# Performance work log

Hardware: AMD Instinct MI355X
Metric: run time of the kernel (lower is better)

## Reference

```python
import jax, jax.numpy as jnp
import numpy as np

B, S, D, H = 2, 2048, 1024, 16
DK = D // H


def setup_inputs() -> dict:
    key = jax.random.key(0)
    ks = jax.random.split(key, 7)
    x = jax.random.normal(ks[0], (B, S, D), dtype=jnp.float32)
    gamma = jax.random.normal(ks[1], (D,), dtype=jnp.float32)
    mask = jax.random.randint(ks[2], (B, S), 0, 2, dtype=jnp.int32)
    w_qkv_w = jax.random.normal(ks[3], (D, 3 * D), dtype=jnp.float32) / np.sqrt(D)
    w_qkv_b = jax.random.normal(ks[4], (3 * D,), dtype=jnp.float32) * 0.02
    w_o_w = jax.random.normal(ks[5], (D, D), dtype=jnp.float32) / np.sqrt(D)
    w_o_b = jax.random.normal(ks[6], (D,), dtype=jnp.float32) * 0.02
    return {"x": x, "gamma": gamma, "mask": mask, "w_qkv_w": w_qkv_w,
            "w_qkv_b": w_qkv_b, "w_o_w": w_o_w, "w_o_b": w_o_b}


def reference(x, gamma, mask, w_qkv_w, w_qkv_b, w_o_w, w_o_b):
    b, s, d = x.shape
    # QKV projection, then per-head interleaved chunk (matches torch view+chunk)
    qkv = x @ w_qkv_w + w_qkv_b                      # [B,S,3D]
    qkv = qkv.reshape(b, s, H, 3 * DK).transpose(0, 2, 1, 3)  # [B,H,S,3*dk]
    q, k, v = jnp.split(qkv, 3, axis=-1)             # each [B,H,S,dk]
    scale = 1.0 / np.sqrt(DK).astype(np.float32)
    scores = jnp.einsum('bhqd,bhkd->bhqk', q, k) * scale  # [B,H,S,S]
    m = mask[:, None, None, :]                       # 2D mask -> [B,1,1,S]
    scores = jnp.where(m == 0, -jnp.inf, scores)
    attn = jax.nn.softmax(scores, axis=-1)           # dropout p=0.0 -> identity
    out = jnp.einsum('bhqk,bhkd->bhqd', attn, v)     # [B,H,S,dk]
    out = out.transpose(0, 2, 1, 3).reshape(b, s, d) # [B,S,D]
    out = out @ w_o_w + w_o_b
    return (gamma + 1.0) * out
```

## Files before the change

### kernel.cpp

```cpp
#include <hip/hip_runtime.h>
#include <hip/hip_bf16.h>


using bf16 = __hip_bfloat16;
typedef __attribute__((ext_vector_type(8))) short bf16x8;
typedef __attribute__((ext_vector_type(4))) float f32x4;

#define QSCALE 0.18033688011112042f

static __device__ __forceinline__ f32x4 mfma_bf16(bf16x8 a, bf16x8 b, f32x4 c) {
    return __builtin_amdgcn_mfma_f32_16x16x32_bf16(a, b, c, 0, 0, 0);
}

static __device__ __forceinline__ void gld_lds16(const void* g, void* s) {
    __builtin_amdgcn_global_load_lds(
        (const __attribute__((address_space(1))) unsigned int*)g,
        (__attribute__((address_space(3))) unsigned int*)s,
        16, 0, 0);
}

static __device__ __forceinline__ short f2s(float f) {
    bf16 h = __float2bfloat16(f);
    return *reinterpret_cast<short*>(&h);
}

__global__ void prep_kernel(const float* __restrict__ x, bf16* __restrict__ xb,
                            const float* __restrict__ wqkv, bf16* __restrict__ wqkvT,
                            const float* __restrict__ wo, bf16* __restrict__ woT) {
    __shared__ float tile[32][33];
    int blk = blockIdx.x;
    if (blk < 4096) {
        int i = blk * 256 + threadIdx.x;
        float4 f = reinterpret_cast<const float4*>(x)[i];
        xb[4*i+0] = __float2bfloat16(f.x);
        xb[4*i+1] = __float2bfloat16(f.y);
        xb[4*i+2] = __float2bfloat16(f.z);
        xb[4*i+3] = __float2bfloat16(f.w);
        return;
    }
    const float* in; bf16* out; int R, C, bx, by;
    if (blk < 7168) {
        int idx = blk - 4096; in = wqkv; out = wqkvT; R = 1024; C = 3072;
        bx = idx % 96; by = idx / 96;
    } else {
        int idx = blk - 7168; in = wo; out = woT; R = 1024; C = 1024;
        bx = idx & 31; by = idx >> 5;
    }
    int c0 = bx * 32, r0 = by * 32;
    int xo = threadIdx.x & 31, yo = threadIdx.x >> 5;
#pragma unroll
    for (int i = 0; i < 32; i += 8) tile[yo + i][xo] = in[(size_t)(r0 + yo + i) * C + c0 + xo];
    __syncthreads();
#pragma unroll
    for (int i = 0; i < 32; i += 8)
        out[(size_t)(c0 + yo + i) * R + r0 + xo] = __float2bfloat16(tile[xo][yo + i]);
}

__global__ void transpose_v_kernel(const bf16* __restrict__ in, bf16* __restrict__ out) {
    __shared__ bf16 t[64][72];
    const int bh = blockIdx.y, s0 = blockIdx.x * 64;
    const int r = threadIdx.x >> 2, c16 = (threadIdx.x & 3) * 16;
    const uint4* src = (const uint4*)(in + ((size_t)bh * 2048 + s0 + r) * 64 + c16);
    uint4 a0 = src[0], a1 = src[1];
    *(uint4*)&t[r][c16] = a0;
    *(uint4*)&t[r][c16 + 8] = a1;
    __syncthreads();
    bf16 tmp[16];
#pragma unroll
    for (int ii = 0; ii < 16; ++ii) {
        int i = c16 + ii;
        int a = i >> 5, rem = i & 31, q = rem >> 3, jj = rem & 7;
        int sp = a * 32 + q * 4 + (jj < 4 ? jj : 16 + jj - 4);
        tmp[ii] = t[sp][r];
    }
    uint4* dst = (uint4*)(out + ((size_t)bh * 64 + r) * 2048 + s0 + c16);
    dst[0] = ((uint4*)tmp)[0];
    dst[1] = ((uint4*)tmp)[1];
}

template <int EPI, int TM, int MINW>
__global__ __launch_bounds__(256, MINW)
void gemm_bt_kernel(const bf16* __restrict__ A, const bf16* __restrict__ Bt,
                    int M, int N, int K,
                    const float* __restrict__ bias, const float* __restrict__ gamma,
                    bf16* __restrict__ Qout, bf16* __restrict__ Kout, bf16* __restrict__ Vout,
                    float* __restrict__ Cout) {
    constexpr int MI = TM / 32;
    constexpr int CA = TM / 32;
    __shared__ __align__(16) bf16 As[TM * 64];
    __shared__ __align__(16) bf16 Bs[128 * 64];

    const int tid  = threadIdx.x;
    const int wave = tid >> 6, lane = tid & 63;
    const int quad = lane >> 4, l16 = lane & 15;
    const int wr = wave >> 1, wc = wave & 1;
    const int bm = blockIdx.y, bn = blockIdx.x;

    f32x4 acc[MI][4] = {};

    const int crow = lane >> 3;
    const int sblk = (lane & 7) ^ (crow & 7);
    const bf16* gA[CA]; const bf16* gB[4]; bf16* lA[CA]; bf16* lB[4];
#pragma unroll
    for (int c = 0; c < CA; ++c) {
        int ch = wave * CA + c;
        gA[c] = A + (size_t)(bm * TM + ch * 8 + crow) * K + sblk * 8;
        lA[c] = As + ch * 512 + lane * 8;
    }
#pragma unroll
    for (int c = 0; c < 4; ++c) {
        int ch = wave * 4 + c;
        gB[c] = Bt + (size_t)(bn * 128 + ch * 8 + crow) * K + sblk * 8;
        lB[c] = Bs + ch * 512 + lane * 8;
    }
    const int xr = l16 & 7;

    for (int k0 = 0; k0 < K; k0 += 64) {
#pragma unroll
        for (int c = 0; c < CA; ++c) gld_lds16(gA[c] + k0, lA[c]);
#pragma unroll
        for (int c = 0; c < 4; ++c) gld_lds16(gB[c] + k0, lB[c]);
        __syncthreads();
#pragma unroll
        for (int ks = 0; ks < 2; ++ks) {
            bf16x8 af[MI], bfr[4];
#pragma unroll
            for (int mi = 0; mi < MI; ++mi)
                af[mi] = *(const bf16x8*)(As + (wr * (TM/2) + mi * 16 + l16) * 64 + ((4 * ks + quad) ^ xr) * 8);
#pragma unroll
            for (int ni = 0; ni < 4; ++ni)
                bfr[ni] = *(const bf16x8*)(Bs + (wc * 64 + ni * 16 + l16) * 64 + ((4 * ks + quad) ^ xr) * 8);
#pragma unroll
            for (int mi = 0; mi < MI; ++mi)
#pragma unroll
                for (int ni = 0; ni < 4; ++ni)
                    acc[mi][ni] = mfma_bf16(af[mi], bfr[ni], acc[mi][ni]);
        }
        __syncthreads();
    }

#pragma unroll
    for (int mi = 0; mi < MI; ++mi) {
#pragma unroll
        for (int ni = 0; ni < 4; ++ni) {
#pragma unroll
            for (int r = 0; r < 4; ++r) {
                int row = bm * TM + wr * (TM/2) + mi * 16 + quad * 4 + r;
                int col = bn * 128 + wc * 64 + ni * 16 + l16;
                float v = acc[mi][ni][r];
                if (EPI == 0) {
                    v += bias[col];
                    int h = col / 192;
                    int rr = col - h * 192;
                    int which = rr >> 6, dk = rr & 63;
                    int b = row >> 11, s = row & 2047;
                    size_t bh = (size_t)b * 16 + h;
                    if (which == 0) {
                        Qout[(bh * 2048 + s) * 64 + dk] = __float2bfloat16(v * QSCALE);
                    } else if (which == 1) {
                        Kout[(bh * 2048 + s) * 64 + dk] = __float2bfloat16(v);
                    } else {
                        Vout[(bh * 2048 + s) * 64 + dk] = __float2bfloat16(v);
                    }
                } else {
                    float o = (gamma[col] + 1.0f) * (v + bias[col]);
                    Cout[(size_t)row * N + col] = o;
                }
            }
        }
    }
}

__global__ __launch_bounds__(128, 1)
void attn_kernel(const bf16* __restrict__ Qb, const bf16* __restrict__ Kb,
                 const bf16* __restrict__ Vtp, const int* __restrict__ mask,
                 bf16* __restrict__ Aout) {
    __shared__ __align__(16) bf16 Ks[2][64 * 64];
    __shared__ __align__(16) bf16 Vs[2][64 * 64];
    __shared__ float Biass[2][64];

    const int bh = blockIdx.y;
    const int b = bh >> 4, h = bh & 15;
    const int q0 = blockIdx.x * 128;
    const int tid = threadIdx.x;
    const int wave = tid >> 6, lane = tid & 63;
    const int quad = lane >> 4, l16 = lane & 15;
    const int xr = l16 & 7;

    bf16x8 aq[4][2];
#pragma unroll
    for (int m = 0; m < 4; ++m) {
        const bf16* qp = Qb + ((size_t)bh * 2048 + q0 + wave * 64 + m * 16 + l16) * 64;
        aq[m][0] = *(const bf16x8*)(qp + quad * 8);
        aq[m][1] = *(const bf16x8*)(qp + 32 + quad * 8);
    }

    bf16x8 ones;
#pragma unroll
    for (int j = 0; j < 8; ++j) ones[j] = (short)0x3F80;

    f32x4 O[4][4] = {};
    f32x4 Lacc[4] = {};

    const int r8 = lane >> 3, b8 = lane & 7;
    const int srcb = b8 ^ r8;
    const bf16* gK = Kb  + ((size_t)bh * 2048 + wave * 8 + r8) * 64 + srcb * 8;
    const bf16* gV = Vtp + ((size_t)bh * 64 + wave * 8 + r8) * 2048 + srcb * 8;
    bf16* lK[2][4]; bf16* lV[2][4];
#pragma unroll
    for (int p = 0; p < 2; ++p)
#pragma unroll
        for (int c = 0; c < 4; ++c) {
            lK[p][c] = Ks[p] + c * 1024 + wave * 512 + lane * 8;
            lV[p][c] = Vs[p] + c * 1024 + wave * 512 + lane * 8;
        }

    int mreg = 0;
#pragma unroll
    for (int c = 0; c < 4; ++c) {
        gld_lds16(gK + c * 1024, lK[0][c]);
        gld_lds16(gV + (size_t)c * 32768, lV[0][c]);
    }
    if (tid < 64) {
        Biass[0][tid] = mask[b * 2048 + tid] ? -24.0f : -1e30f;
        mreg = mask[b * 2048 + 64 + tid];
    }

    for (int kt = 0; kt < 32; ++kt) {
        __syncthreads();
        const int cur = kt & 1, nxt = cur ^ 1;

        if (kt + 1 < 32) {
#pragma unroll
            for (int c = 0; c < 4; ++c) {
                gld_lds16(gK + (size_t)(kt + 1) * 4096 + c * 1024, lK[nxt][c]);
                gld_lds16(gV + (kt + 1) * 64 + (size_t)c * 32768, lV[nxt][c]);
            }
            if (tid < 64) Biass[nxt][tid] = mreg ? -24.0f : -1e30f;
        }
        if (kt + 2 < 32 && tid < 64) mreg = mask[b * 2048 + (kt + 2) * 64 + tid];

        f32x4 bias4[4];
        bf16x8 bk[4][2];
#pragma unroll
        for (int kt4 = 0; kt4 < 4; ++kt4) {
            bias4[kt4] = *(const f32x4*)(&Biass[cur][0] + kt4 * 16 + quad * 4);
            const bf16* kp = Ks[cur] + (kt4 * 16 + l16) * 64;
            bk[kt4][0] = *(const bf16x8*)(kp + (quad ^ xr) * 8);
            bk[kt4][1] = *(const bf16x8*)(kp + ((quad + 4) ^ xr) * 8);
        }
        bf16x8 bv8[2][4];
#pragma unroll
        for (int a = 0; a < 2; ++a)
#pragma unroll
            for (int nt = 0; nt < 4; ++nt)
                bv8[a][nt] = *(const bf16x8*)(Vs[cur] + (nt * 16 + l16) * 64 + ((a * 4 + quad) ^ xr) * 8);

#pragma unroll
        for (int m = 0; m < 4; ++m) {
            f32x4 sv[4];
#pragma unroll
            for (int kt4 = 0; kt4 < 4; ++kt4) {
                f32x4 c = {0.f, 0.f, 0.f, 0.f};
                c = mfma_bf16(bk[kt4][0], aq[m][0], c);
                c = mfma_bf16(bk[kt4][1], aq[m][1], c);
                sv[kt4] = c;
            }
            float p[4][4];
#pragma unroll
            for (int kt4 = 0; kt4 < 4; ++kt4)
#pragma unroll
                for (int r = 0; r < 4; ++r)
                    p[kt4][r] = __builtin_amdgcn_exp2f(sv[kt4][r] + bias4[kt4][r]);

#pragma unroll
            for (int a = 0; a < 2; ++a) {
                bf16x8 pa;
                pa[0] = f2s(p[2*a][0]);   pa[1] = f2s(p[2*a][1]);
                pa[2] = f2s(p[2*a][2]);   pa[3] = f2s(p[2*a][3]);
                pa[4] = f2s(p[2*a+1][0]); pa[5] = f2s(p[2*a+1][1]);
                pa[6] = f2s(p[2*a+1][2]); pa[7] = f2s(p[2*a+1][3]);
                Lacc[m] = mfma_bf16(pa, ones, Lacc[m]);
#pragma unroll
                for (int nt = 0; nt < 4; ++nt)
                    O[m][nt] = mfma_bf16(pa, bv8[a][nt], O[m][nt]);
            }
        }
    }

#pragma unroll
    for (int m = 0; m < 4; ++m) {
        float inv[4];
#pragma unroll
        for (int r = 0; r < 4; ++r) inv[r] = __builtin_amdgcn_rcpf(Lacc[m][r]);
#pragma unroll
        for (int nt = 0; nt < 4; ++nt) {
#pragma unroll
            for (int r = 0; r < 4; ++r) {
                int row = q0 + wave * 64 + m * 16 + quad * 4 + r;
                Aout[((size_t)b * 2048 + row) * 1024 + h * 64 + nt * 16 + l16] =
                    __float2bfloat16(O[m][nt][r] * inv[r]);
            }
        }
    }
}

extern "C" void kernel_launch(void* const* d_in, const int* in_sizes, int n_in,
                              void* d_out, int out_size, void* d_ws, size_t ws_size,
                              hipStream_t stream) {
    const float* x     = (const float*)d_in[0];
    const float* gamma = (const float*)d_in[1];
    const int*   mask  = (const int*)d_in[2];
    const float* wqkv  = (const float*)d_in[3];
    const float* bqkv  = (const float*)d_in[4];
    const float* wo    = (const float*)d_in[5];
    const float* bo    = (const float*)d_in[6];
    float* out = (float*)d_out;

    char* ws = (char*)d_ws;
    const size_t MB = 1u << 20;
    bf16* xb    = (bf16*)(ws);
    bf16* wqkvT = (bf16*)(ws + 8 * MB);
    bf16* woT   = (bf16*)(ws + 14 * MB);
    bf16* Qb    = (bf16*)(ws + 16 * MB);
    bf16* Kb    = (bf16*)(ws + 24 * MB);
    bf16* Vt    = (bf16*)(ws + 32 * MB);
    bf16* Vtmp  = (bf16*)(ws + 40 * MB);
    bf16* attn  = (bf16*)(ws + 40 * MB);

    prep_kernel<<<8192, 256, 0, stream>>>(x, xb, wqkv, wqkvT, wo, woT);

    gemm_bt_kernel<0, 128, 3><<<dim3(24, 32), 256, 0, stream>>>(
        xb, wqkvT, 4096, 3072, 1024, bqkv, nullptr, Qb, Kb, Vtmp, nullptr);

    transpose_v_kernel<<<dim3(32, 32), 256, 0, stream>>>(Vtmp, Vt);

    attn_kernel<<<dim3(16, 32), 128, 0, stream>>>(Qb, Kb, Vt, mask, attn);

    gemm_bt_kernel<1, 64, 4><<<dim3(8, 64), 256, 0, stream>>>(
        attn, woT, 4096, 1024, 1024, bo, gamma, nullptr, nullptr, nullptr, out);
}
```

Baseline: 188.8 us.

## Split attention key range across wave pairs and permute QKV weights for coalesced epilogue

The attention kernel now runs 256 threads per block. Two wave pairs each process half of the key sequence and merge their partial O and row sums through LDS at the end, which doubles in-flight waves per query tile. The QKV weight transpose now reorders output columns into Q/K/V-major order and folds the Q scale in. This simplifies the GEMM epilogue to one destination and one bias load per column. Probability packing to bf16 uses a round-add plus a byte permute instead of the per-element conversion, which adds rounding differences and uses more LDS per block.

Result: slower. 200.1 us (+6.0%).

```diff
diff --git a/kernel.cpp b/kernel.cpp
--- a/kernel.cpp
+++ b/kernel.cpp
@@ -19,9 +19,10 @@
         16, 0, 0);
 }
 
-static __device__ __forceinline__ short f2s(float f) {
-    bf16 h = __float2bfloat16(f);
-    return *reinterpret_cast<short*>(&h);
+static __device__ __forceinline__ unsigned int pk_bf16(float lo, float hi) {
+    unsigned int ul = __builtin_bit_cast(unsigned int, lo) + 0x8000u;
+    unsigned int uh = __builtin_bit_cast(unsigned int, hi) + 0x8000u;
+    return __builtin_amdgcn_perm(uh, ul, 0x07060302u);
 }
 
 __global__ void prep_kernel(const float* __restrict__ x, bf16* __restrict__ xb,
@@ -38,22 +39,34 @@
         xb[4*i+3] = __float2bfloat16(f.w);
         return;
     }
-    const float* in; bf16* out; int R, C, bx, by;
+    int xo = threadIdx.x & 31, yo = threadIdx.x >> 5;
     if (blk < 7168) {
-        int idx = blk - 4096; in = wqkv; out = wqkvT; R = 1024; C = 3072;
-        bx = idx % 96; by = idx / 96;
+        int idx = blk - 4096;
+        int c0 = (idx % 96) * 32, r0 = (idx / 96) * 32;
+#pragma unroll
+        for (int i = 0; i < 32; i += 8)
+            tile[yo + i][xo] = wqkv[(size_t)(r0 + yo + i) * 3072 + c0 + xo];
+        __syncthreads();
+#pragma unroll
+        for (int i = 0; i < 32; i += 8) {
+            int c = c0 + yo + i;
+            int hh = c / 192, rem = c - hh * 192;
+            int which = rem >> 6, dk = rem & 63;
+            int rowp = which * 1024 + hh * 64 + dk;
+            float sc = (which == 0) ? QSCALE : 1.0f;
+            wqkvT[(size_t)rowp * 1024 + r0 + xo] = __float2bfloat16(tile[xo][yo + i] * sc);
+        }
     } else {
-        int idx = blk - 7168; in = wo; out = woT; R = 1024; C = 1024;
-        bx = idx & 31; by = idx >> 5;
-    }
-    int c0 = bx * 32, r0 = by * 32;
-    int xo = threadIdx.x & 31, yo = threadIdx.x >> 5;
-#pragma unroll
-    for (int i = 0; i < 32; i += 8) tile[yo + i][xo] = in[(size_t)(r0 + yo + i) * C + c0 + xo];
-    __syncthreads();
-#pragma unroll
-    for (int i = 0; i < 32; i += 8)
-        out[(size_t)(c0 + yo + i) * R + r0 + xo] = __float2bfloat16(tile[xo][yo + i]);
+        int idx = blk - 7168;
+        int c0 = (idx & 31) * 32, r0 = (idx >> 5) * 32;
+#pragma unroll
+        for (int i = 0; i < 32; i += 8)
+            tile[yo + i][xo] = wo[(size_t)(r0 + yo + i) * 1024 + c0 + xo];
+        __syncthreads();
+#pragma unroll
+        for (int i = 0; i < 32; i += 8)
+            woT[(size_t)(c0 + yo + i) * 1024 + r0 + xo] = __float2bfloat16(tile[xo][yo + i]);
+    }
 }
 
 __global__ void transpose_v_kernel(const bf16* __restrict__ in, bf16* __restrict__ out) {
@@ -143,41 +156,39 @@
     for (int mi = 0; mi < MI; ++mi) {
 #pragma unroll
         for (int ni = 0; ni < 4; ++ni) {
-#pragma unroll
-            for (int r = 0; r < 4; ++r) {
-                int row = bm * TM + wr * (TM/2) + mi * 16 + quad * 4 + r;
-                int col = bn * 128 + wc * 64 + ni * 16 + l16;
-                float v = acc[mi][ni][r];
-                if (EPI == 0) {
-                    v += bias[col];
-                    int h = col / 192;
-                    int rr = col - h * 192;
-                    int which = rr >> 6, dk = rr & 63;
+            int col = bn * 128 + wc * 64 + ni * 16 + l16;
+            if (EPI == 0) {
+                int which = col >> 10, hh = (col >> 6) & 15, dk = col & 63;
+                float bsc = (which == 0) ? QSCALE : 1.0f;
+                float bv = bias[hh * 192 + which * 64 + dk] * bsc;
+                bf16* dst = (which == 0) ? Qout : ((which == 1) ? Kout : Vout);
+#pragma unroll
+                for (int r = 0; r < 4; ++r) {
+                    int row = bm * TM + wr * (TM/2) + mi * 16 + quad * 4 + r;
                     int b = row >> 11, s = row & 2047;
-                    size_t bh = (size_t)b * 16 + h;
-                    if (which == 0) {
-                        Qout[(bh * 2048 + s) * 64 + dk] = __float2bfloat16(v * QSCALE);
-                    } else if (which == 1) {
-                        Kout[(bh * 2048 + s) * 64 + dk] = __float2bfloat16(v);
-                    } else {
-                        Vout[(bh * 2048 + s) * 64 + dk] = __float2bfloat16(v);
-                    }
-                } else {
-                    float o = (gamma[col] + 1.0f) * (v + bias[col]);
-                    Cout[(size_t)row * N + col] = o;
+                    dst[(((size_t)b * 16 + hh) * 2048 + s) * 64 + dk] =
+                        __float2bfloat16(acc[mi][ni][r] + bv);
                 }
-            }
-        }
-    }
-}
-
-__global__ __launch_bounds__(128, 1)
+            } else {
+                float g1 = gamma[col] + 1.0f, bv = bias[col];
+#pragma unroll
+                for (int r = 0; r < 4; ++r) {
+                    int row = bm * TM + wr * (TM/2) + mi * 16 + quad * 4 + r;
+                    Cout[(size_t)row * N + col] = g1 * (acc[mi][ni][r] + bv);
+                }
+            }
+        }
+    }
+}
+
+__global__ __launch_bounds__(256, 2)
 void attn_kernel(const bf16* __restrict__ Qb, const bf16* __restrict__ Kb,
                  const bf16* __restrict__ Vtp, const int* __restrict__ mask,
                  bf16* __restrict__ Aout) {
-    __shared__ __align__(16) bf16 Ks[2][64 * 64];
-    __shared__ __align__(16) bf16 Vs[2][64 * 64];
-    __shared__ float Biass[2][64];
+    __shared__ __align__(16) unsigned char smem[66560];
+    bf16* KsB = (bf16*)smem;
+    bf16* VsB = (bf16*)(smem + 32768);
+    float* BiasB = (float*)(smem + 65536);
 
     const int bh = blockIdx.y;
     const int b = bh >> 4, h = bh & 15;
@@ -186,11 +197,12 @@
     const int wave = tid >> 6, lane = tid & 63;
     const int quad = lane >> 4, l16 = lane & 15;
     const int xr = l16 & 7;
+    const int qw = wave & 1, kh = wave >> 1;
 
     bf16x8 aq[4][2];
 #pragma unroll
     for (int m = 0; m < 4; ++m) {
-        const bf16* qp = Qb + ((size_t)bh * 2048 + q0 + wave * 64 + m * 16 + l16) * 64;
+        const bf16* qp = Qb + ((size_t)bh * 2048 + q0 + qw * 64 + m * 16 + l16) * 64;
         aq[m][0] = *(const bf16x8*)(qp + quad * 8);
         aq[m][1] = *(const bf16x8*)(qp + 32 + quad * 8);
     }
@@ -204,15 +216,15 @@
 
     const int r8 = lane >> 3, b8 = lane & 7;
     const int srcb = b8 ^ r8;
-    const bf16* gK = Kb  + ((size_t)bh * 2048 + wave * 8 + r8) * 64 + srcb * 8;
-    const bf16* gV = Vtp + ((size_t)bh * 64 + wave * 8 + r8) * 2048 + srcb * 8;
+    const bf16* gK = Kb  + ((size_t)bh * 2048 + kh * 1024 + qw * 8 + r8) * 64 + srcb * 8;
+    const bf16* gV = Vtp + ((size_t)bh * 64 + qw * 8 + r8) * 2048 + kh * 1024 + srcb * 8;
     bf16* lK[2][4]; bf16* lV[2][4];
 #pragma unroll
     for (int p = 0; p < 2; ++p)
 #pragma unroll
         for (int c = 0; c < 4; ++c) {
-            lK[p][c] = Ks[p] + c * 1024 + wave * 512 + lane * 8;
-            lV[p][c] = Vs[p] + c * 1024 + wave * 512 + lane * 8;
+            lK[p][c] = KsB + (kh * 2 + p) * 4096 + c * 1024 + qw * 512 + lane * 8;
+            lV[p][c] = VsB + (kh * 2 + p) * 4096 + c * 1024 + qw * 512 + lane * 8;
         }
 
     int mreg = 0;
@@ -221,31 +233,35 @@
         gld_lds16(gK + c * 1024, lK[0][c]);
         gld_lds16(gV + (size_t)c * 32768, lV[0][c]);
     }
-    if (tid < 64) {
-        Biass[0][tid] = mask[b * 2048 + tid] ? -24.0f : -1e30f;
-        mreg = mask[b * 2048 + 64 + tid];
-    }
-
-    for (int kt = 0; kt < 32; ++kt) {
+    if (qw == 0) {
+        BiasB[(kh * 2) * 64 + lane] = mask[b * 2048 + kh * 1024 + lane] ? -24.0f : -1e30f;
+        mreg = mask[b * 2048 + kh * 1024 + 64 + lane];
+    }
+
+    for (int kt = 0; kt < 16; ++kt) {
         __syncthreads();
         const int cur = kt & 1, nxt = cur ^ 1;
 
-        if (kt + 1 < 32) {
+        if (kt + 1 < 16) {
 #pragma unroll
             for (int c = 0; c < 4; ++c) {
                 gld_lds16(gK + (size_t)(kt + 1) * 4096 + c * 1024, lK[nxt][c]);
                 gld_lds16(gV + (kt + 1) * 64 + (size_t)c * 32768, lV[nxt][c]);
             }
-            if (tid < 64) Biass[nxt][tid] = mreg ? -24.0f : -1e30f;
-        }
-        if (kt + 2 < 32 && tid < 64) mreg = mask[b * 2048 + (kt + 2) * 64 + tid];
+            if (qw == 0) BiasB[(kh * 2 + nxt) * 64 + lane] = mreg ? -24.0f : -1e30f;
+        }
+        if (kt + 2 < 16 && qw == 0) mreg = mask[b * 2048 + kh * 1024 + (kt + 2) * 64 + lane];
+
+        const bf16* Ksc = KsB + (kh * 2 + cur) * 4096;
+        const bf16* Vsc = VsB + (kh * 2 + cur) * 4096;
+        const float* Bic = BiasB + (kh * 2 + cur) * 64;
 
         f32x4 bias4[4];
         bf16x8 bk[4][2];
 #pragma unroll
         for (int kt4 = 0; kt4 < 4; ++kt4) {
-            bias4[kt4] = *(const f32x4*)(&Biass[cur][0] + kt4 * 16 + quad * 4);
-            const bf16* kp = Ks[cur] + (kt4 * 16 + l16) * 64;
+            bias4[kt4] = *(const f32x4*)(Bic + kt4 * 16 + quad * 4);
+            const bf16* kp = Ksc + (kt4 * 16 + l16) * 64;
             bk[kt4][0] = *(const bf16x8*)(kp + (quad ^ xr) * 8);
             bk[kt4][1] = *(const bf16x8*)(kp + ((quad + 4) ^ xr) * 8);
         }
@@ -254,7 +270,7 @@
         for (int a = 0; a < 2; ++a)
 #pragma unroll
             for (int nt = 0; nt < 4; ++nt)
-                bv8[a][nt] = *(const bf16x8*)(Vs[cur] + (nt * 16 + l16) * 64 + ((a * 4 + quad) ^ xr) * 8);
+                bv8[a][nt] = *(const bf16x8*)(Vsc + (nt * 16 + l16) * 64 + ((a * 4 + quad) ^ xr) * 8);
 
 #pragma unroll
         for (int m = 0; m < 4; ++m) {
@@ -275,11 +291,12 @@
 
 #pragma unroll
             for (int a = 0; a < 2; ++a) {
-                bf16x8 pa;
-                pa[0] = f2s(p[2*a][0]);   pa[1] = f2s(p[2*a][1]);
-                pa[2] = f2s(p[2*a][2]);   pa[3] = f2s(p[2*a][3]);
-                pa[4] = f2s(p[2*a+1][0]); pa[5] = f2s(p[2*a+1][1]);
-                pa[6] = f2s(p[2*a+1][2]); pa[7] = f2s(p[2*a+1][3]);
+                uint4 uv;
+                uv.x = pk_bf16(p[2*a][0],   p[2*a][1]);
+                uv.y = pk_bf16(p[2*a][2],   p[2*a][3]);
+                uv.z = pk_bf16(p[2*a+1][0], p[2*a+1][1]);
+                uv.w = pk_bf16(p[2*a+1][2], p[2*a+1][3]);
+                bf16x8 pa = __builtin_bit_cast(bf16x8, uv);
                 Lacc[m] = mfma_bf16(pa, ones, Lacc[m]);
 #pragma unroll
                 for (int nt = 0; nt < 4; ++nt)
@@ -288,18 +305,44 @@
         }
     }
 
-#pragma unroll
-    for (int m = 0; m < 4; ++m) {
-        float inv[4];
-#pragma unroll
-        for (int r = 0; r < 4; ++r) inv[r] = __builtin_amdgcn_rcpf(Lacc[m][r]);
-#pragma unroll
-        for (int nt = 0; nt < 4; ++nt) {
-#pragma unroll
-            for (int r = 0; r < 4; ++r) {
-                int row = q0 + wave * 64 + m * 16 + quad * 4 + r;
-                Aout[((size_t)b * 2048 + row) * 1024 + h * 64 + nt * 16 + l16] =
-                    __float2bfloat16(O[m][nt][r] * inv[r]);
+    __syncthreads();
+    float* mg = (float*)smem;
+    float* mp = mg + (qw * 64 + lane) * 81;
+    if (kh == 1) {
+#pragma unroll
+        for (int m = 0; m < 4; ++m) {
+#pragma unroll
+            for (int nt = 0; nt < 4; ++nt)
+#pragma unroll
+                for (int r = 0; r < 4; ++r) mp[m * 16 + nt * 4 + r] = O[m][nt][r];
+#pragma unroll
+            for (int r = 0; r < 4; ++r) mp[64 + m * 4 + r] = Lacc[m][r];
+        }
+    }
+    __syncthreads();
+    if (kh == 0) {
+#pragma unroll
+        for (int m = 0; m < 4; ++m) {
+#pragma unroll
+            for (int nt = 0; nt < 4; ++nt)
+#pragma unroll
+                for (int r = 0; r < 4; ++r) O[m][nt][r] += mp[m * 16 + nt * 4 + r];
+#pragma unroll
+            for (int r = 0; r < 4; ++r) Lacc[m][r] += mp[64 + m * 4 + r];
+        }
+#pragma unroll
+        for (int m = 0; m < 4; ++m) {
+            float inv[4];
+#pragma unroll
+            for (int r = 0; r < 4; ++r) inv[r] = __builtin_amdgcn_rcpf(Lacc[m][r]);
+#pragma unroll
+            for (int nt = 0; nt < 4; ++nt) {
+#pragma unroll
+                for (int r = 0; r < 4; ++r) {
+                    int row = q0 + qw * 64 + m * 16 + quad * 4 + r;
+                    Aout[((size_t)b * 2048 + row) * 1024 + h * 64 + nt * 16 + l16] =
+                        __float2bfloat16(O[m][nt][r] * inv[r]);
+                }
             }
         }
     }
@@ -335,7 +378,7 @@
 
     transpose_v_kernel<<<dim3(32, 32), 256, 0, stream>>>(Vtmp, Vt);
 
-    attn_kernel<<<dim3(16, 32), 128, 0, stream>>>(Qb, Kb, Vt, mask, attn);
+    attn_kernel<<<dim3(16, 32), 256, 0, stream>>>(Qb, Kb, Vt, mask, attn);
 
     gemm_bt_kernel<1, 64, 4><<<dim3(8, 64), 256, 0, stream>>>(
         attn, woT, 4096, 1024, 1024, bo, gamma, nullptr, nullptr, nullptr, out);
```

## Process two K/V subtiles per barrier and pack bf16 probabilities via byte-perm

Applied to the files above, without the earlier changes.

Each pipeline step of the attention kernel now stages 128 keys (two 64-key subtiles) in double-buffered LDS, halving the number of block barriers and loop iterations. All threads now fill the mask bias buffer instead of only the first wave. The float-to-bf16 conversion of softmax probabilities is replaced with a round-half-up add plus a v_perm packing two values per instruction, which is cheaper than round-to-nearest-even but rounds slightly differently. LDS use doubles, which the kernel's single-block-per-CU launch bounds can afford.

Result: slower. 203.5 us (+7.8%).

```diff
diff --git a/kernel.cpp b/kernel.cpp
--- a/kernel.cpp
+++ b/kernel.cpp
@@ -19,9 +19,10 @@
         16, 0, 0);
 }
 
-static __device__ __forceinline__ short f2s(float f) {
-    bf16 h = __float2bfloat16(f);
-    return *reinterpret_cast<short*>(&h);
+static __device__ __forceinline__ unsigned int pk_bf16(float lo, float hi) {
+    unsigned int ul = __builtin_bit_cast(unsigned int, lo) + 0x8000u;
+    unsigned int uh = __builtin_bit_cast(unsigned int, hi) + 0x8000u;
+    return __builtin_amdgcn_perm(uh, ul, 0x07060302u);
 }
 
 __global__ void prep_kernel(const float* __restrict__ x, bf16* __restrict__ xb,
@@ -175,9 +176,9 @@
 void attn_kernel(const bf16* __restrict__ Qb, const bf16* __restrict__ Kb,
                  const bf16* __restrict__ Vtp, const int* __restrict__ mask,
                  bf16* __restrict__ Aout) {
-    __shared__ __align__(16) bf16 Ks[2][64 * 64];
-    __shared__ __align__(16) bf16 Vs[2][64 * 64];
-    __shared__ float Biass[2][64];
+    __shared__ __align__(16) bf16 Ks[2][2][64 * 64];
+    __shared__ __align__(16) bf16 Vs[2][2][64 * 64];
+    __shared__ float Biass[2][128];
 
     const int bh = blockIdx.y;
     const int b = bh >> 4, h = bh & 15;
@@ -206,84 +207,93 @@
     const int srcb = b8 ^ r8;
     const bf16* gK = Kb  + ((size_t)bh * 2048 + wave * 8 + r8) * 64 + srcb * 8;
     const bf16* gV = Vtp + ((size_t)bh * 64 + wave * 8 + r8) * 2048 + srcb * 8;
-    bf16* lK[2][4]; bf16* lV[2][4];
-#pragma unroll
-    for (int p = 0; p < 2; ++p)
+
+    auto lK = [&](int p, int s, int c) {
+        return Ks[p][s] + c * 1024 + wave * 512 + lane * 8;
+    };
+    auto lV = [&](int p, int s, int c) {
+        return Vs[p][s] + c * 1024 + wave * 512 + lane * 8;
+    };
+
+    int mreg = 0;
+#pragma unroll
+    for (int s = 0; s < 2; ++s)
 #pragma unroll
         for (int c = 0; c < 4; ++c) {
-            lK[p][c] = Ks[p] + c * 1024 + wave * 512 + lane * 8;
-            lV[p][c] = Vs[p] + c * 1024 + wave * 512 + lane * 8;
-        }
-
-    int mreg = 0;
-#pragma unroll
-    for (int c = 0; c < 4; ++c) {
-        gld_lds16(gK + c * 1024, lK[0][c]);
-        gld_lds16(gV + (size_t)c * 32768, lV[0][c]);
-    }
-    if (tid < 64) {
-        Biass[0][tid] = mask[b * 2048 + tid] ? -24.0f : -1e30f;
-        mreg = mask[b * 2048 + 64 + tid];
-    }
-
-    for (int kt = 0; kt < 32; ++kt) {
+            gld_lds16(gK + (size_t)(s * 64) * 64 + c * 1024, lK(0, s, c));
+            gld_lds16(gV + s * 64 + (size_t)c * 32768, lV(0, s, c));
+        }
+    Biass[0][wave * 64 + lane] = mask[b * 2048 + wave * 64 + lane] ? -24.0f : -1e30f;
+    mreg = mask[b * 2048 + 128 + wave * 64 + lane];
+
+    for (int kt = 0; kt < 16; ++kt) {
         __syncthreads();
         const int cur = kt & 1, nxt = cur ^ 1;
 
-        if (kt + 1 < 32) {
-#pragma unroll
-            for (int c = 0; c < 4; ++c) {
-                gld_lds16(gK + (size_t)(kt + 1) * 4096 + c * 1024, lK[nxt][c]);
-                gld_lds16(gV + (kt + 1) * 64 + (size_t)c * 32768, lV[nxt][c]);
+        if (kt + 1 < 16) {
+#pragma unroll
+            for (int s = 0; s < 2; ++s)
+#pragma unroll
+                for (int c = 0; c < 4; ++c) {
+                    gld_lds16(gK + (size_t)((kt + 1) * 128 + s * 64) * 64 + c * 1024, lK(nxt, s, c));
+                    gld_lds16(gV + (kt + 1) * 128 + s * 64 + (size_t)c * 32768, lV(nxt, s, c));
+                }
+            Biass[nxt][wave * 64 + lane] = mreg ? -24.0f : -1e30f;
+        }
+        if (kt + 2 < 16) mreg = mask[b * 2048 + (kt + 2) * 128 + wave * 64 + lane];
+
+#pragma unroll
+        for (int s = 0; s < 2; ++s) {
+            const bf16* Ksc = Ks[cur][s];
+            const bf16* Vsc = Vs[cur][s];
+            const float* Bic = &Biass[cur][s * 64];
+
+            f32x4 bias4[4];
+            bf16x8 bk[4][2];
+#pragma unroll
+            for (int kt4 = 0; kt4 < 4; ++kt4) {
+                bias4[kt4] = *(const f32x4*)(Bic + kt4 * 16 + quad * 4);
+                const bf16* kp = Ksc + (kt4 * 16 + l16) * 64;
+                bk[kt4][0] = *(const bf16x8*)(kp + (quad ^ xr) * 8);
+                bk[kt4][1] = *(const bf16x8*)(kp + ((quad + 4) ^ xr) * 8);
             }
-            if (tid < 64) Biass[nxt][tid] = mreg ? -24.0f : -1e30f;
-        }
-        if (kt + 2 < 32 && tid < 64) mreg = mask[b * 2048 + (kt + 2) * 64 + tid];
-
-        f32x4 bias4[4];
-        bf16x8 bk[4][2];
-#pragma unroll
-        for (int kt4 = 0; kt4 < 4; ++kt4) {
-            bias4[kt4] = *(const f32x4*)(&Biass[cur][0] + kt4 * 16 + quad * 4);
-            const bf16* kp = Ks[cur] + (kt4 * 16 + l16) * 64;
-            bk[kt4][0] = *(const bf16x8*)(kp + (quad ^ xr) * 8);
-            bk[kt4][1] = *(const bf16x8*)(kp + ((quad + 4) ^ xr) * 8);
-        }
-        bf16x8 bv8[2][4];
-#pragma unroll
-        for (int a = 0; a < 2; ++a)
-#pragma unroll
-            for (int nt = 0; nt < 4; ++nt)
-                bv8[a][nt] = *(const bf16x8*)(Vs[cur] + (nt * 16 + l16) * 64 + ((a * 4 + quad) ^ xr) * 8);
-
-#pragma unroll
-        for (int m = 0; m < 4; ++m) {
-            f32x4 sv[4];
-#pragma unroll
-            for (int kt4 = 0; kt4 < 4; ++kt4) {
-                f32x4 c = {0.f, 0.f, 0.f, 0.f};
-                c = mfma_bf16(bk[kt4][0], aq[m][0], c);
-                c = mfma_bf16(bk[kt4][1], aq[m][1], c);
-                sv[kt4] = c;
-            }
-            float p[4][4];
-#pragma unroll
-            for (int kt4 = 0; kt4 < 4; ++kt4)
-#pragma unroll
-                for (int r = 0; r < 4; ++r)
-                    p[kt4][r] = __builtin_amdgcn_exp2f(sv[kt4][r] + bias4[kt4][r]);
-
-#pragma unroll
-            for (int a = 0; a < 2; ++a) {
-                bf16x8 pa;
-                pa[0] = f2s(p[2*a][0]);   pa[1] = f2s(p[2*a][1]);
-                pa[2] = f2s(p[2*a][2]);   pa[3] = f2s(p[2*a][3]);
-                pa[4] = f2s(p[2*a+1][0]); pa[5] = f2s(p[2*a+1][1]);
-                pa[6] = f2s(p[2*a+1][2]); pa[7] = f2s(p[2*a+1][3]);
-                Lacc[m] = mfma_bf16(pa, ones, Lacc[m]);
+            bf16x8 bv8[2][4];
+#pragma unroll
+            for (int a = 0; a < 2; ++a)
 #pragma unroll
                 for (int nt = 0; nt < 4; ++nt)
-                    O[m][nt] = mfma_bf16(pa, bv8[a][nt], O[m][nt]);
+                    bv8[a][nt] = *(const bf16x8*)(Vsc + (nt * 16 + l16) * 64 + ((a * 4 + quad) ^ xr) * 8);
+
+#pragma unroll
+            for (int m = 0; m < 4; ++m) {
+                f32x4 sv[4];
+#pragma unroll
+                for (int kt4 = 0; kt4 < 4; ++kt4) {
+                    f32x4 c = {0.f, 0.f, 0.f, 0.f};
+                    c = mfma_bf16(bk[kt4][0], aq[m][0], c);
+                    c = mfma_bf16(bk[kt4][1], aq[m][1], c);
+                    sv[kt4] = c;
+                }
+                float p[4][4];
+#pragma unroll
+                for (int kt4 = 0; kt4 < 4; ++kt4)
+#pragma unroll
+                    for (int r = 0; r < 4; ++r)
+                        p[kt4][r] = __builtin_amdgcn_exp2f(sv[kt4][r] + bias4[kt4][r]);
+
+#pragma unroll
+                for (int a = 0; a < 2; ++a) {
+                    uint4 uv;
+                    uv.x = pk_bf16(p[2*a][0],   p[2*a][1]);
+                    uv.y = pk_bf16(p[2*a][2],   p[2*a][3]);
+                    uv.z = pk_bf16(p[2*a+1][0], p[2*a+1][1]);
+                    uv.w = pk_bf16(p[2*a+1][2], p[2*a+1][3]);
+                    bf16x8 pa = __builtin_bit_cast(bf16x8, uv);
+                    Lacc[m] = mfma_bf16(pa, ones, Lacc[m]);
+#pragma unroll
+                    for (int nt = 0; nt < 4; ++nt)
+                        O[m][nt] = mfma_bf16(pa, bv8[a][nt], O[m][nt]);
+                }
             }
         }
     }
```
